# Optimization experiments

Hardware: AMD Instinct MI355X
Metric: run time of the kernel (lower is better)

The kernel has to match this reference:

```python
import jax, jax.numpy as jnp
import numpy as np

TOPK, NC, ALPHA, BETA, EPS = 13, 80, 1.0, 6.0, 1e-9


def make_anchors():
    # YOLOv8 anchor centers for a 640x640 image, strides 8/16/32 -> 8400 points
    pts = []
    for s in (8, 16, 32):
        n = 640 // s
        yv, xv = jnp.meshgrid(jnp.arange(n, dtype=jnp.float32) + 0.5,
                              jnp.arange(n, dtype=jnp.float32) + 0.5, indexing='ij')
        pts.append(jnp.stack([xv, yv], -1).reshape(-1, 2) * s)
    return jnp.concatenate(pts, 0)  # (8400, 2)


def setup_inputs() -> dict:
    key = jax.random.key(0)
    ks = jax.random.split(key, 5)
    B, NMAX = 32, 64
    anc_points = make_anchors()
    A = anc_points.shape[0]
    pd_scores = jax.random.uniform(ks[0], (B, A, NC), jnp.float32)
    # predicted boxes: anchor-centered xyxy with random extents
    half = jax.random.uniform(ks[1], (B, A, 2), jnp.float32) * 32.0 + 2.0
    ctr = anc_points[None]
    pd_bboxes = jnp.concatenate([ctr - half, ctr + half], -1)
    # gt boxes: valid xyxy inside the 640x640 image
    xy = jax.random.uniform(ks[2], (B, NMAX, 2), jnp.float32) * 520.0
    wh = jax.random.uniform(ks[3], (B, NMAX, 2), jnp.float32) * 120.0 + 8.0
    gt_bboxes = jnp.concatenate([xy, xy + wh], -1)
    gt_labels = jax.random.randint(ks[4], (B, NMAX, 1), 0, NC).astype(jnp.int64)
    mask_gt = jnp.ones((B, NMAX, 1), jnp.float32)
    return {"pd_scores": pd_scores, "pd_bboxes": pd_bboxes, "anc_points": anc_points,
            "gt_labels": gt_labels, "gt_bboxes": gt_bboxes, "mask_gt": mask_gt}


def _iou_xyxy(box1, box2, eps=1e-7):
    # box1: (B, N, 1, 4), box2: (B, 1, A, 4) -> iou (B, N, A)
    lt = jnp.maximum(box1[..., :2], box2[..., :2])
    rb = jnp.minimum(box1[..., 2:], box2[..., 2:])
    wh = jnp.clip(rb - lt, 0.0)
    inter = wh[..., 0] * wh[..., 1]
    a1 = (box1[..., 2] - box1[..., 0]) * (box1[..., 3] - box1[..., 1])
    a2 = (box2[..., 2] - box2[..., 0]) * (box2[..., 3] - box2[..., 1])
    return inter / (a1 + a2 - inter + eps)


def reference(pd_scores, pd_bboxes, anc_points, gt_labels, gt_bboxes, mask_gt):
    B, A, _ = pd_scores.shape
    N = gt_bboxes.shape[1]
    # --- select_candidates_in_gts: anchor center strictly inside gt box ---
    deltas = jnp.concatenate([
        anc_points[None, None] - gt_bboxes[:, :, None, :2],
        gt_bboxes[:, :, None, 2:] - anc_points[None, None]], -1)  # (B,N,A,4)
    mask_in_gts = (deltas.min(-1) > EPS).astype(jnp.float32)       # (B,N,A)
    mask_valid = mask_in_gts * mask_gt                             # mask_gt (B,N,1)
    # --- get_box_metrics ---
    # bbox_scores[b,n,a] = pd_scores[b, a, gt_labels[b,n]]
    bbox_scores = jnp.take_along_axis(pd_scores.transpose(0, 2, 1),
                                      gt_labels, axis=1)           # (B,N,A)
    overlaps = jnp.clip(_iou_xyxy(gt_bboxes[:, :, None], pd_bboxes[:, None]), 0.0)
    align_metric = (bbox_scores ** ALPHA) * (overlaps ** BETA)
    align_metric = align_metric * mask_valid
    overlaps = overlaps * mask_valid
    # --- select_topk_candidates ---
    _, topk_idxs = jax.lax.top_k(align_metric, TOPK)               # (B,N,TOPK)
    bi = jnp.arange(B)[:, None, None]
    ni = jnp.arange(N)[None, :, None]
    mask_topk = jnp.zeros_like(align_metric).at[bi, ni, topk_idxs].set(1.0)
    mask_pos = mask_valid * mask_topk                              # (B,N,A)
    fg_mask = mask_pos.sum(1)                                      # (B,A)
    # multi-GT conflict resolution (always applied; no-op when no conflicts)
    max_metric = align_metric.max(1, keepdims=True)
    mask_pos = jnp.where(fg_mask[:, None, :] > 1,
                         mask_pos * (align_metric == max_metric).astype(mask_pos.dtype),
                         mask_pos)
    fg_mask = mask_pos.sum(1)
    target_gt_idx = jnp.argmax(mask_pos, 1)                        # (B,A)
    # --- targets ---
    b2 = jnp.arange(B)[:, None]
    target_labels = gt_labels[..., 0][b2, target_gt_idx]           # (B,A)
    target_bboxes = gt_bboxes[b2, target_gt_idx]                   # (B,A,4)
    pos_align = (align_metric * mask_pos).max(1)                   # (B,A)
    target_scores = jax.nn.one_hot(target_labels, NC, dtype=jnp.float32) \
        * pos_align[..., None]                                     # (B,A,NC)
    return (target_bboxes, target_scores, fg_mask.astype(bool))
```

## Files before the change

kernel.cpp:

```cpp
#include <hip/hip_runtime.h>

#define BB 32
#define AA 8400
#define NGT 64
#define NCLS 80
#define TOPK 13
#define SLOTS 5
#define CHUNK 256
#define NCHUNK 33

__device__ __forceinline__ void anchor_xy(int a, float& px, float& py) {
    if (a < 6400)      { int y = a / 80;          int x = a - 80 * y;  px = (x + 0.5f) * 8.0f;  py = (y + 0.5f) * 8.0f; }
    else if (a < 8000) { int r = a - 6400; int y = r / 40; int x = r - 40 * y; px = (x + 0.5f) * 16.0f; py = (y + 0.5f) * 16.0f; }
    else               { int r = a - 8000; int y = r / 20; int x = r - 20 * y; px = (x + 0.5f) * 32.0f; py = (y + 0.5f) * 32.0f; }
}

__global__ __launch_bounds__(256) void k_topk(
    const float* __restrict__ pd_scores,
    const float4* __restrict__ pd_bboxes,
    const int* __restrict__ gt_labels,
    const float4* __restrict__ gt_bboxes,
    const float* __restrict__ mask_gt,
    int* __restrict__ list)
{
    __shared__ unsigned long long keys[4 * TOPK];
    int tid = threadIdx.x;
    int w = tid >> 6, lane = tid & 63;
    int gid = blockIdx.x * 2 + (w >> 1);
    int half = w & 1;
    int b = gid >> 6;

    if (tid < 4 * TOPK) keys[tid] = 0;
    __syncthreads();

    float4 g = gt_bboxes[gid];
    int label = gt_labels[gid];
    float ga1 = (g.z - g.x) * (g.w - g.y);
    bool valid = mask_gt[gid] > 0.0f;

    float va[SLOTS]; int ai[SLOTS]; int cnt = 0;
    #pragma unroll
    for (int j = 0; j < SLOTS; ++j) { va[j] = -1.0f; ai[j] = -1; }

#define SCAN_LEVEL(S, N, OFF)                                                   \
    {                                                                           \
        const float inv = 1.0f / (float)(S);                                    \
        int xlo = (int)floorf(g.x * inv - 0.5f); if (xlo < 0) xlo = 0;          \
        int xhi = (int)ceilf (g.z * inv - 0.5f); if (xhi > (N)-1) xhi = (N)-1;  \
        int ylo = (int)floorf(g.y * inv - 0.5f); if (ylo < 0) ylo = 0;          \
        int yhi = (int)ceilf (g.w * inv - 0.5f); if (yhi > (N)-1) yhi = (N)-1;  \
        int nx = xhi - xlo + 1, ny = yhi - ylo + 1;                             \
        int tot = (nx > 0 && ny > 0) ? nx * ny : 0;                             \
        for (int c = half * 64 + lane; c < tot; c += 128) {                     \
            int yy = c / nx, xx = c - yy * nx;                                  \
            int gx = xlo + xx, gy = ylo + yy;                                   \
            int a = (OFF) + gy * (N) + gx;                                      \
            float px = (gx + 0.5f) * (float)(S), py = (gy + 0.5f) * (float)(S); \
            float dmin = fminf(fminf(px - g.x, py - g.y),                       \
                               fminf(g.z - px, g.w - py));                      \
            if (dmin > 1e-9f) {                                                 \
                float4 pb = pd_bboxes[b * AA + a];                              \
                float ltx = fmaxf(g.x, pb.x), lty = fmaxf(g.y, pb.y);           \
                float rbx = fminf(g.z, pb.z), rby = fminf(g.w, pb.w);           \
                float wd = fmaxf(rbx - ltx, 0.0f), hg = fmaxf(rby - lty, 0.0f); \
                float inter = wd * hg;                                          \
                float a2 = (pb.z - pb.x) * (pb.w - pb.y);                       \
                float iou = fmaxf(inter / (ga1 + a2 - inter + 1e-7f), 0.0f);    \
                float sc = pd_scores[(size_t)(b * AA + a) * NCLS + label];      \
                float i2 = iou * iou;                                           \
                float v = sc * (i2 * i2 * i2);                                  \
                if (v > 0.0f) {                                                 \
                    _Pragma("unroll")                                           \
                    for (int j = 0; j < SLOTS; ++j)                             \
                        if (j == cnt) { va[j] = v; ai[j] = a; }                 \
                    cnt++;                                                      \
                }                                                               \
            }                                                                   \
        }                                                                       \
    }

    if (valid) {
        SCAN_LEVEL(8, 80, 0)
        SCAN_LEVEL(16, 40, 6400)
        SCAN_LEVEL(32, 20, 8000)
    }
#undef SCAN_LEVEL

    for (int k = 0; k < TOPK; ++k) {
        unsigned long long key = 0;
        #pragma unroll
        for (int j = 0; j < SLOTS; ++j)
            if (va[j] > 0.0f) {
                unsigned long long kk =
                    ((unsigned long long)__float_as_uint(va[j]) << 32)
                    | (unsigned)(0x7FFFFFFF - ai[j]);
                key = kk > key ? kk : key;
            }
        #pragma unroll
        for (int off = 32; off; off >>= 1) {
            unsigned long long o = __shfl_xor(key, off);
            key = o > key ? o : key;
        }
        if (key == 0) break;
        if (lane == 0) keys[w * TOPK + k] = key;
        int wa = 0x7FFFFFFF - (int)(unsigned)(key & 0xFFFFFFFFull);
        #pragma unroll
        for (int j = 0; j < SLOTS; ++j) if (ai[j] == wa) va[j] = -1.0f;
    }

    __syncthreads();

    if (!(w & 1)) {
        unsigned long long mykey = (lane < 2 * TOPK) ? keys[w * TOPK + lane] : 0;
        int kc = 0;
        for (int k = 0; k < TOPK; ++k) {
            unsigned long long best = mykey;
            #pragma unroll
            for (int off = 32; off; off >>= 1) {
                unsigned long long o = __shfl_xor(best, off);
                best = o > best ? o : best;
            }
            if (best == 0) break;
            if (lane == 0)
                list[gid * 16 + k] = 0x7FFFFFFF - (int)(unsigned)(best & 0xFFFFFFFFull);
            kc++;
            if (mykey == best) mykey = 0;
        }
        if (lane == 0)
            for (int k = kc; k < 16; ++k) list[gid * 16 + k] = -1;
    }
}

__global__ __launch_bounds__(256) void k_out(
    const float* __restrict__ pd_scores,
    const float4* __restrict__ pd_bboxes,
    const int* __restrict__ gt_labels,
    const float4* __restrict__ gt_bboxes,
    const float* __restrict__ mask_gt,
    const int* __restrict__ list,
    float4* __restrict__ out_bbox,
    float* __restrict__ out_fg,
    float4* __restrict__ out_scores)
{
    __shared__ unsigned int s_lo[CHUNK], s_hi[CHUNK];
    __shared__ float4 s_gt[NGT];
    __shared__ int    s_glab[NGT];
    __shared__ float  s_gmsk[NGT];

    int bidx = blockIdx.x;
    int b = bidx / NCHUNK;
    int chunk = bidx - b * NCHUNK;
    int abase = chunk * CHUNK;
    int count = AA - abase; if (count > CHUNK) count = CHUNK;
    int tid = threadIdx.x;

    float4* dst = out_scores + (size_t)(b * AA + abase) * (NCLS / 4);
    const float4 z4 = make_float4(0.f, 0.f, 0.f, 0.f);
    for (int ci = tid; ci < count * (NCLS / 4); ci += 256)
        dst[ci] = z4;

    s_lo[tid] = 0; s_hi[tid] = 0;
    if (tid < NGT) {
        s_gt[tid]   = gt_bboxes[b * NGT + tid];
        s_glab[tid] = gt_labels[b * NGT + tid];
        s_gmsk[tid] = mask_gt[b * NGT + tid];
    }
    __syncthreads();

    const int* blist = list + b * NGT * 16;
    for (int e = tid; e < NGT * 16; e += 256) {
        int a = blist[e];
        int rel = a - abase;
        if (a >= 0 && rel >= 0 && rel < count) {
            int n = e >> 4;
            if (n < 32) atomicOr(&s_lo[rel], 1u << n);
            else        atomicOr(&s_hi[rel], 1u << (n - 32));
        }
    }
    __syncthreads();

    if (tid < count) {
        int a = abase + tid;
        int idx = b * AA + a;
        unsigned long long m = ((unsigned long long)s_hi[tid] << 32) | s_lo[tid];
        float pos = 0.0f; int tgt = 0; int fg = 0;
        if (m) {
            float px, py; anchor_xy(a, px, py);
            float4 pb = pd_bboxes[idx];
            float a2 = (pb.z - pb.x) * (pb.w - pb.y);
            if (__popcll(m) == 1) {
                int n = __ffsll((unsigned long long)m) - 1;
                float4 gg = s_gt[n];
                float ltx = fmaxf(gg.x, pb.x), lty = fmaxf(gg.y, pb.y);
                float rbx = fminf(gg.z, pb.z), rby = fminf(gg.w, pb.w);
                float wd = fmaxf(rbx - ltx, 0.0f), hg = fmaxf(rby - lty, 0.0f);
                float inter = wd * hg;
                float a1 = (gg.z - gg.x) * (gg.w - gg.y);
                float iou = fmaxf(inter / (a1 + a2 - inter + 1e-7f), 0.0f);
                float sc = pd_scores[(size_t)idx * NCLS + s_glab[n]];
                float i2 = iou * iou;
                pos = sc * (i2 * i2 * i2);
                tgt = n; fg = 1;
            } else {
                float mmax = 0.0f; unsigned long long nb = 0;
                for (int j0 = 0; j0 < NGT; j0 += 8) {
                    float v[8];
                    #pragma unroll
                    for (int j = 0; j < 8; ++j) {
                        int n = j0 + j;
                        float4 gg = s_gt[n];
                        float sc = pd_scores[(size_t)idx * NCLS + s_glab[n]];
                        float dmin = fminf(fminf(px - gg.x, py - gg.y),
                                           fminf(gg.z - px, gg.w - py));
                        float ltx = fmaxf(gg.x, pb.x), lty = fmaxf(gg.y, pb.y);
                        float rbx = fminf(gg.z, pb.z), rby = fminf(gg.w, pb.w);
                        float wd = fmaxf(rbx - ltx, 0.0f), hg = fmaxf(rby - lty, 0.0f);
                        float inter = wd * hg;
                        float a1 = (gg.z - gg.x) * (gg.w - gg.y);
                        float iou = fmaxf(inter / (a1 + a2 - inter + 1e-7f), 0.0f);
                        float i2 = iou * iou;
                        bool ok = (s_gmsk[n] > 0.0f) && (dmin > 1e-9f);
                        v[j] = ok ? sc * (i2 * i2 * i2) : 0.0f;
                    }
                    #pragma unroll
                    for (int j = 0; j < 8; ++j) {
                        int n = j0 + j;
                        float vv = v[j];
                        if (vv > mmax) { mmax = vv; nb = m & (1ull << n); }
                        else if (vv == mmax && vv > 0.0f) nb |= m & (1ull << n);
                    }
                }
                if (nb) { tgt = __ffsll(nb) - 1; pos = mmax; fg = 1; }
            }
        }
        out_bbox[idx] = s_gt[tgt];
        out_fg[idx] = fg ? 1.0f : 0.0f;
        if (fg && pos != 0.0f)
            ((float*)dst)[(size_t)tid * NCLS + s_glab[tgt]] = pos;
    }
}

extern "C" void kernel_launch(void* const* d_in, const int* in_sizes, int n_in,
                              void* d_out, int out_size, void* d_ws, size_t ws_size,
                              hipStream_t stream) {
    const float*  pd_scores = (const float*) d_in[0];
    const float4* pd_bboxes = (const float4*)d_in[1];
    const int*    gt_labels = (const int*)   d_in[3];
    const float4* gt_bboxes = (const float4*)d_in[4];
    const float*  mask_gt   = (const float*) d_in[5];

    float* out = (float*)d_out;
    float4* out_bbox   = (float4*)out;
    float4* out_scores = (float4*)(out + (size_t)BB * AA * 4);
    float*  out_fg     = out + (size_t)BB * AA * 4 + (size_t)BB * AA * NCLS;

    int* list = (int*)d_ws;

    k_topk<<<BB * NGT / 2, 256, 0, stream>>>(pd_scores, pd_bboxes,
                                             gt_labels, gt_bboxes, mask_gt, list);

    k_out<<<BB * NCHUNK, 256, 0, stream>>>(
        pd_scores, pd_bboxes, gt_labels, gt_bboxes, mask_gt, list,
        out_bbox, out_fg, out_scores);
}
```

Before: 68.71 us.

## Move output zero-fill to a separate kernel and scatter top-k hits as global bitmasks

A new fill kernel zeroes the scores, fg and bitmask buffers and writes default bboxes up front. The top-k kernel now atomically ORs each selected GT's bit into a per-anchor 64-bit mask in global memory, replacing the per-GT candidate list. The resolve kernel reads that mask directly and exits early for anchors with no hits, which removes the per-block list scan and shared-memory atomics. The trade-off is an extra kernel launch, a full-size zero pass over the large score tensor in a kernel separate from the resolve work, and global atomics.

```diff
diff --git a/kernel.cpp b/kernel.cpp
--- a/kernel.cpp
+++ b/kernel.cpp
@@ -15,20 +15,36 @@
     else               { int r = a - 8000; int y = r / 20; int x = r - 20 * y; px = (x + 0.5f) * 32.0f; py = (y + 0.5f) * 32.0f; }
 }
 
+__global__ __launch_bounds__(256) void k_fill(
+    float4* __restrict__ scores4,
+    float4* __restrict__ fg4,
+    float4* __restrict__ bbox4,
+    float4* __restrict__ bits4,
+    const float4* __restrict__ gt_bboxes)
+{
+    const int nthr = gridDim.x * 256;
+    int gtid = blockIdx.x * 256 + threadIdx.x;
+    const float4 z4 = make_float4(0.f, 0.f, 0.f, 0.f);
+    for (int j = gtid; j < BB * AA * (NCLS / 4); j += nthr) scores4[j] = z4;
+    for (int j = gtid; j < BB * AA / 4;          j += nthr) fg4[j] = z4;
+    for (int j = gtid; j < BB * AA / 2;          j += nthr) bits4[j] = z4;
+    for (int j = gtid; j < BB * AA;              j += nthr) bbox4[j] = gt_bboxes[(j / AA) << 6];
+}
+
 __global__ __launch_bounds__(256) void k_topk(
     const float* __restrict__ pd_scores,
     const float4* __restrict__ pd_bboxes,
     const int* __restrict__ gt_labels,
     const float4* __restrict__ gt_bboxes,
     const float* __restrict__ mask_gt,
-    int* __restrict__ list)
+    unsigned long long* __restrict__ bits)
 {
     __shared__ unsigned long long keys[4 * TOPK];
     int tid = threadIdx.x;
     int w = tid >> 6, lane = tid & 63;
     int gid = blockIdx.x * 2 + (w >> 1);
     int half = w & 1;
-    int b = gid >> 6;
+    int b = gid >> 6, n = gid & 63;
 
     if (tid < 4 * TOPK) keys[tid] = 0;
     __syncthreads();
@@ -112,7 +128,8 @@
 
     if (!(w & 1)) {
         unsigned long long mykey = (lane < 2 * TOPK) ? keys[w * TOPK + lane] : 0;
-        int kc = 0;
+        unsigned long long* mybits = bits + (size_t)b * AA;
+        unsigned long long nbit = 1ull << n;
         for (int k = 0; k < TOPK; ++k) {
             unsigned long long best = mykey;
             #pragma unroll
@@ -121,28 +138,26 @@
                 best = o > best ? o : best;
             }
             if (best == 0) break;
-            if (lane == 0)
-                list[gid * 16 + k] = 0x7FFFFFFF - (int)(unsigned)(best & 0xFFFFFFFFull);
-            kc++;
+            if (lane == 0) {
+                int wa = 0x7FFFFFFF - (int)(unsigned)(best & 0xFFFFFFFFull);
+                atomicOr(&mybits[wa], nbit);
+            }
             if (mykey == best) mykey = 0;
         }
-        if (lane == 0)
-            for (int k = kc; k < 16; ++k) list[gid * 16 + k] = -1;
-    }
-}
-
-__global__ __launch_bounds__(256) void k_out(
+    }
+}
+
+__global__ __launch_bounds__(256) void k_resolve(
     const float* __restrict__ pd_scores,
     const float4* __restrict__ pd_bboxes,
     const int* __restrict__ gt_labels,
     const float4* __restrict__ gt_bboxes,
     const float* __restrict__ mask_gt,
-    const int* __restrict__ list,
+    const unsigned long long* __restrict__ bits,
     float4* __restrict__ out_bbox,
     float* __restrict__ out_fg,
-    float4* __restrict__ out_scores)
+    float* __restrict__ out_scores)
 {
-    __shared__ unsigned int s_lo[CHUNK], s_hi[CHUNK];
     __shared__ float4 s_gt[NGT];
     __shared__ int    s_glab[NGT];
     __shared__ float  s_gmsk[NGT];
@@ -154,12 +169,6 @@
     int count = AA - abase; if (count > CHUNK) count = CHUNK;
     int tid = threadIdx.x;
 
-    float4* dst = out_scores + (size_t)(b * AA + abase) * (NCLS / 4);
-    const float4 z4 = make_float4(0.f, 0.f, 0.f, 0.f);
-    for (int ci = tid; ci < count * (NCLS / 4); ci += 256)
-        dst[ci] = z4;
-
-    s_lo[tid] = 0; s_hi[tid] = 0;
     if (tid < NGT) {
         s_gt[tid]   = gt_bboxes[b * NGT + tid];
         s_glab[tid] = gt_labels[b * NGT + tid];
@@ -167,77 +176,64 @@
     }
     __syncthreads();
 
-    const int* blist = list + b * NGT * 16;
-    for (int e = tid; e < NGT * 16; e += 256) {
-        int a = blist[e];
-        int rel = a - abase;
-        if (a >= 0 && rel >= 0 && rel < count) {
-            int n = e >> 4;
-            if (n < 32) atomicOr(&s_lo[rel], 1u << n);
-            else        atomicOr(&s_hi[rel], 1u << (n - 32));
-        }
-    }
-    __syncthreads();
-
-    if (tid < count) {
-        int a = abase + tid;
-        int idx = b * AA + a;
-        unsigned long long m = ((unsigned long long)s_hi[tid] << 32) | s_lo[tid];
-        float pos = 0.0f; int tgt = 0; int fg = 0;
-        if (m) {
-            float px, py; anchor_xy(a, px, py);
-            float4 pb = pd_bboxes[idx];
-            float a2 = (pb.z - pb.x) * (pb.w - pb.y);
-            if (__popcll(m) == 1) {
-                int n = __ffsll((unsigned long long)m) - 1;
+    if (tid >= count) return;
+    int a = abase + tid;
+    int idx = b * AA + a;
+    unsigned long long m = bits[idx];
+    if (!m) return;
+
+    float px, py; anchor_xy(a, px, py);
+    float4 pb = pd_bboxes[idx];
+    float a2 = (pb.z - pb.x) * (pb.w - pb.y);
+    float pos = 0.0f; int tgt = 0;
+    if (__popcll(m) == 1) {
+        int n = __ffsll((unsigned long long)m) - 1;
+        float4 gg = s_gt[n];
+        float ltx = fmaxf(gg.x, pb.x), lty = fmaxf(gg.y, pb.y);
+        float rbx = fminf(gg.z, pb.z), rby = fminf(gg.w, pb.w);
+        float wd = fmaxf(rbx - ltx, 0.0f), hg = fmaxf(rby - lty, 0.0f);
+        float inter = wd * hg;
+        float a1 = (gg.z - gg.x) * (gg.w - gg.y);
+        float iou = fmaxf(inter / (a1 + a2 - inter + 1e-7f), 0.0f);
+        float sc = pd_scores[(size_t)idx * NCLS + s_glab[n]];
+        float i2 = iou * iou;
+        pos = sc * (i2 * i2 * i2);
+        tgt = n;
+    } else {
+        float mmax = 0.0f; unsigned long long nb = 0;
+        for (int j0 = 0; j0 < NGT; j0 += 8) {
+            float v[8];
+            #pragma unroll
+            for (int j = 0; j < 8; ++j) {
+                int n = j0 + j;
                 float4 gg = s_gt[n];
+                float sc = pd_scores[(size_t)idx * NCLS + s_glab[n]];
+                float dmin = fminf(fminf(px - gg.x, py - gg.y),
+                                   fminf(gg.z - px, gg.w - py));
                 float ltx = fmaxf(gg.x, pb.x), lty = fmaxf(gg.y, pb.y);
                 float rbx = fminf(gg.z, pb.z), rby = fminf(gg.w, pb.w);
                 float wd = fmaxf(rbx - ltx, 0.0f), hg = fmaxf(rby - lty, 0.0f);
                 float inter = wd * hg;
                 float a1 = (gg.z - gg.x) * (gg.w - gg.y);
                 float iou = fmaxf(inter / (a1 + a2 - inter + 1e-7f), 0.0f);
-                float sc = pd_scores[(size_t)idx * NCLS + s_glab[n]];
                 float i2 = iou * iou;
-                pos = sc * (i2 * i2 * i2);
-                tgt = n; fg = 1;
-            } else {
-                float mmax = 0.0f; unsigned long long nb = 0;
-                for (int j0 = 0; j0 < NGT; j0 += 8) {
-                    float v[8];
-                    #pragma unroll
-                    for (int j = 0; j < 8; ++j) {
-                        int n = j0 + j;
-                        float4 gg = s_gt[n];
-                        float sc = pd_scores[(size_t)idx * NCLS + s_glab[n]];
-                        float dmin = fminf(fminf(px - gg.x, py - gg.y),
-                                           fminf(gg.z - px, gg.w - py));
-                        float ltx = fmaxf(gg.x, pb.x), lty = fmaxf(gg.y, pb.y);
-                        float rbx = fminf(gg.z, pb.z), rby = fminf(gg.w, pb.w);
-                        float wd = fmaxf(rbx - ltx, 0.0f), hg = fmaxf(rby - lty, 0.0f);
-                        float inter = wd * hg;
-                        float a1 = (gg.z - gg.x) * (gg.w - gg.y);
-                        float iou = fmaxf(inter / (a1 + a2 - inter + 1e-7f), 0.0f);
-                        float i2 = iou * iou;
-                        bool ok = (s_gmsk[n] > 0.0f) && (dmin > 1e-9f);
-                        v[j] = ok ? sc * (i2 * i2 * i2) : 0.0f;
-                    }
-                    #pragma unroll
-                    for (int j = 0; j < 8; ++j) {
-                        int n = j0 + j;
-                        float vv = v[j];
-                        if (vv > mmax) { mmax = vv; nb = m & (1ull << n); }
-                        else if (vv == mmax && vv > 0.0f) nb |= m & (1ull << n);
-                    }
-                }
-                if (nb) { tgt = __ffsll(nb) - 1; pos = mmax; fg = 1; }
+                bool ok = (s_gmsk[n] > 0.0f) && (dmin > 1e-9f);
+                v[j] = ok ? sc * (i2 * i2 * i2) : 0.0f;
+            }
+            #pragma unroll
+            for (int j = 0; j < 8; ++j) {
+                int n = j0 + j;
+                float vv = v[j];
+                if (vv > mmax) { mmax = vv; nb = m & (1ull << n); }
+                else if (vv == mmax && vv > 0.0f) nb |= m & (1ull << n);
             }
         }
-        out_bbox[idx] = s_gt[tgt];
-        out_fg[idx] = fg ? 1.0f : 0.0f;
-        if (fg && pos != 0.0f)
-            ((float*)dst)[(size_t)tid * NCLS + s_glab[tgt]] = pos;
-    }
+        if (!nb) return;
+        tgt = __ffsll(nb) - 1; pos = mmax;
+    }
+    out_bbox[idx] = s_gt[tgt];
+    out_fg[idx] = 1.0f;
+    out_scores[(size_t)idx * NCLS + s_glab[tgt]] = pos;
 }
 
 extern "C" void kernel_launch(void* const* d_in, const int* in_sizes, int n_in,
@@ -251,15 +247,18 @@
 
     float* out = (float*)d_out;
     float4* out_bbox   = (float4*)out;
-    float4* out_scores = (float4*)(out + (size_t)BB * AA * 4);
+    float*  out_scores = out + (size_t)BB * AA * 4;
     float*  out_fg     = out + (size_t)BB * AA * 4 + (size_t)BB * AA * NCLS;
 
-    int* list = (int*)d_ws;
+    unsigned long long* bits = (unsigned long long*)d_ws;
+
+    k_fill<<<2048, 256, 0, stream>>>(
+        (float4*)out_scores, (float4*)out_fg, out_bbox, (float4*)bits, gt_bboxes);
 
     k_topk<<<BB * NGT / 2, 256, 0, stream>>>(pd_scores, pd_bboxes,
-                                             gt_labels, gt_bboxes, mask_gt, list);
-
-    k_out<<<BB * NCHUNK, 256, 0, stream>>>(
-        pd_scores, pd_bboxes, gt_labels, gt_bboxes, mask_gt, list,
+                                             gt_labels, gt_bboxes, mask_gt, bits);
+
+    k_resolve<<<BB * NCHUNK, 256, 0, stream>>>(
+        pd_scores, pd_bboxes, gt_labels, gt_bboxes, mask_gt, bits,
         out_bbox, out_fg, out_scores);
 }
```

After: 77.29 us. +12.5%, slower.

## Split score writing into separate dense one-hot kernel via workspace

Applied to the files above, without the earlier changes.

Moves the target_scores writing out of the resolve kernel. The resolve kernel now stores the per-anchor positive value and label into workspace, and a new elementwise kernel writes each float4 of the (B,A,80) score tensor once, with the value placed in the label slot. This replaces a zero-fill followed by a scattered store with one fully coalesced write pass. It costs an extra kernel launch and a small workspace round-trip.

```diff
diff --git a/kernel.cpp b/kernel.cpp
--- a/kernel.cpp
+++ b/kernel.cpp
@@ -131,7 +131,7 @@
     }
 }
 
-__global__ __launch_bounds__(256) void k_out(
+__global__ __launch_bounds__(256) void k_resolve(
     const float* __restrict__ pd_scores,
     const float4* __restrict__ pd_bboxes,
     const int* __restrict__ gt_labels,
@@ -140,7 +140,8 @@
     const int* __restrict__ list,
     float4* __restrict__ out_bbox,
     float* __restrict__ out_fg,
-    float4* __restrict__ out_scores)
+    float* __restrict__ ws_pos,
+    int* __restrict__ ws_lab)
 {
     __shared__ unsigned int s_lo[CHUNK], s_hi[CHUNK];
     __shared__ float4 s_gt[NGT];
@@ -153,11 +154,6 @@
     int abase = chunk * CHUNK;
     int count = AA - abase; if (count > CHUNK) count = CHUNK;
     int tid = threadIdx.x;
-
-    float4* dst = out_scores + (size_t)(b * AA + abase) * (NCLS / 4);
-    const float4 z4 = make_float4(0.f, 0.f, 0.f, 0.f);
-    for (int ci = tid; ci < count * (NCLS / 4); ci += 256)
-        dst[ci] = z4;
 
     s_lo[tid] = 0; s_hi[tid] = 0;
     if (tid < NGT) {
@@ -179,65 +175,85 @@
     }
     __syncthreads();
 
-    if (tid < count) {
-        int a = abase + tid;
-        int idx = b * AA + a;
-        unsigned long long m = ((unsigned long long)s_hi[tid] << 32) | s_lo[tid];
-        float pos = 0.0f; int tgt = 0; int fg = 0;
-        if (m) {
-            float px, py; anchor_xy(a, px, py);
-            float4 pb = pd_bboxes[idx];
-            float a2 = (pb.z - pb.x) * (pb.w - pb.y);
-            if (__popcll(m) == 1) {
-                int n = __ffsll((unsigned long long)m) - 1;
-                float4 gg = s_gt[n];
-                float ltx = fmaxf(gg.x, pb.x), lty = fmaxf(gg.y, pb.y);
-                float rbx = fminf(gg.z, pb.z), rby = fminf(gg.w, pb.w);
-                float wd = fmaxf(rbx - ltx, 0.0f), hg = fmaxf(rby - lty, 0.0f);
-                float inter = wd * hg;
-                float a1 = (gg.z - gg.x) * (gg.w - gg.y);
-                float iou = fmaxf(inter / (a1 + a2 - inter + 1e-7f), 0.0f);
-                float sc = pd_scores[(size_t)idx * NCLS + s_glab[n]];
-                float i2 = iou * iou;
-                pos = sc * (i2 * i2 * i2);
-                tgt = n; fg = 1;
-            } else {
-                float mmax = 0.0f; unsigned long long nb = 0;
-                for (int j0 = 0; j0 < NGT; j0 += 8) {
-                    float v[8];
-                    #pragma unroll
-                    for (int j = 0; j < 8; ++j) {
-                        int n = j0 + j;
-                        float4 gg = s_gt[n];
-                        float sc = pd_scores[(size_t)idx * NCLS + s_glab[n]];
-                        float dmin = fminf(fminf(px - gg.x, py - gg.y),
-                                           fminf(gg.z - px, gg.w - py));
-                        float ltx = fmaxf(gg.x, pb.x), lty = fmaxf(gg.y, pb.y);
-                        float rbx = fminf(gg.z, pb.z), rby = fminf(gg.w, pb.w);
-                        float wd = fmaxf(rbx - ltx, 0.0f), hg = fmaxf(rby - lty, 0.0f);
-                        float inter = wd * hg;
-                        float a1 = (gg.z - gg.x) * (gg.w - gg.y);
-                        float iou = fmaxf(inter / (a1 + a2 - inter + 1e-7f), 0.0f);
-                        float i2 = iou * iou;
-                        bool ok = (s_gmsk[n] > 0.0f) && (dmin > 1e-9f);
-                        v[j] = ok ? sc * (i2 * i2 * i2) : 0.0f;
-                    }
-                    #pragma unroll
-                    for (int j = 0; j < 8; ++j) {
-                        int n = j0 + j;
-                        float vv = v[j];
-                        if (vv > mmax) { mmax = vv; nb = m & (1ull << n); }
-                        else if (vv == mmax && vv > 0.0f) nb |= m & (1ull << n);
-                    }
+    if (tid >= count) return;
+    int a = abase + tid;
+    int idx = b * AA + a;
+    unsigned long long m = ((unsigned long long)s_hi[tid] << 32) | s_lo[tid];
+    float pos = 0.0f; int tgt = 0; int fg = 0;
+    if (m) {
+        float px, py; anchor_xy(a, px, py);
+        float4 pb = pd_bboxes[idx];
+        float a2 = (pb.z - pb.x) * (pb.w - pb.y);
+        if (__popcll(m) == 1) {
+            int n = __ffsll((unsigned long long)m) - 1;
+            float4 gg = s_gt[n];
+            float ltx = fmaxf(gg.x, pb.x), lty = fmaxf(gg.y, pb.y);
+            float rbx = fminf(gg.z, pb.z), rby = fminf(gg.w, pb.w);
+            float wd = fmaxf(rbx - ltx, 0.0f), hg = fmaxf(rby - lty, 0.0f);
+            float inter = wd * hg;
+            float a1 = (gg.z - gg.x) * (gg.w - gg.y);
+            float iou = fmaxf(inter / (a1 + a2 - inter + 1e-7f), 0.0f);
+            float sc = pd_scores[(size_t)idx * NCLS + s_glab[n]];
+            float i2 = iou * iou;
+            pos = sc * (i2 * i2 * i2);
+            tgt = n; fg = 1;
+        } else {
+            float mmax = 0.0f; unsigned long long nb = 0;
+            for (int j0 = 0; j0 < NGT; j0 += 8) {
+                float v[8];
+                #pragma unroll
+                for (int j = 0; j < 8; ++j) {
+                    int n = j0 + j;
+                    float4 gg = s_gt[n];
+                    float sc = pd_scores[(size_t)idx * NCLS + s_glab[n]];
+                    float dmin = fminf(fminf(px - gg.x, py - gg.y),
+                                       fminf(gg.z - px, gg.w - py));
+                    float ltx = fmaxf(gg.x, pb.x), lty = fmaxf(gg.y, pb.y);
+                    float rbx = fminf(gg.z, pb.z), rby = fminf(gg.w, pb.w);
+                    float wd = fmaxf(rbx - ltx, 0.0f), hg = fmaxf(rby - lty, 0.0f);
+                    float inter = wd * hg;
+                    float a1 = (gg.z - gg.x) * (gg.w - gg.y);
+                    float iou = fmaxf(inter / (a1 + a2 - inter + 1e-7f), 0.0f);
+                    float i2 = iou * iou;
+                    bool ok = (s_gmsk[n] > 0.0f) && (dmin > 1e-9f);
+                    v[j] = ok ? sc * (i2 * i2 * i2) : 0.0f;
                 }
-                if (nb) { tgt = __ffsll(nb) - 1; pos = mmax; fg = 1; }
+                #pragma unroll
+                for (int j = 0; j < 8; ++j) {
+                    int n = j0 + j;
+                    float vv = v[j];
+                    if (vv > mmax) { mmax = vv; nb = m & (1ull << n); }
+                    else if (vv == mmax && vv > 0.0f) nb |= m & (1ull << n);
+                }
             }
-        }
-        out_bbox[idx] = s_gt[tgt];
-        out_fg[idx] = fg ? 1.0f : 0.0f;
-        if (fg && pos != 0.0f)
-            ((float*)dst)[(size_t)tid * NCLS + s_glab[tgt]] = pos;
-    }
+            if (nb) { tgt = __ffsll(nb) - 1; pos = mmax; fg = 1; }
+            else    { pos = 0.0f; tgt = 0; fg = 0; }
+        }
+    }
+    out_bbox[idx] = s_gt[tgt];
+    out_fg[idx] = fg ? 1.0f : 0.0f;
+    ws_pos[idx] = fg ? pos : 0.0f;
+    ws_lab[idx] = s_glab[tgt];
+}
+
+__global__ __launch_bounds__(256) void k_scores(
+    const float* __restrict__ ws_pos,
+    const int* __restrict__ ws_lab,
+    float4* __restrict__ out_scores)
+{
+    int t = blockIdx.x * 256 + threadIdx.x;
+    int anchor = t / (NCLS / 4);
+    int c0 = (t - anchor * (NCLS / 4)) * 4;
+    float pos = ws_pos[anchor];
+    int lab = ws_lab[anchor];
+    float4 r = make_float4(0.0f, 0.0f, 0.0f, 0.0f);
+    if (pos != 0.0f) {
+        if (lab == c0)     r.x = pos;
+        if (lab == c0 + 1) r.y = pos;
+        if (lab == c0 + 2) r.z = pos;
+        if (lab == c0 + 3) r.w = pos;
+    }
+    out_scores[t] = r;
 }
 
 extern "C" void kernel_launch(void* const* d_in, const int* in_sizes, int n_in,
@@ -251,15 +267,20 @@
 
     float* out = (float*)d_out;
     float4* out_bbox   = (float4*)out;
-    float4* out_scores = (float4*)(out + (size_t)BB * AA * 4);
+    float*  out_scores = out + (size_t)BB * AA * 4;
     float*  out_fg     = out + (size_t)BB * AA * 4 + (size_t)BB * AA * NCLS;
 
-    int* list = (int*)d_ws;
+    int*   list   = (int*)d_ws;
+    float* ws_pos = (float*)((char*)d_ws + 131072);
+    int*   ws_lab = (int*)  ((char*)d_ws + 131072 + BB * AA * 4);
 
     k_topk<<<BB * NGT / 2, 256, 0, stream>>>(pd_scores, pd_bboxes,
                                              gt_labels, gt_bboxes, mask_gt, list);
 
-    k_out<<<BB * NCHUNK, 256, 0, stream>>>(
+    k_resolve<<<BB * NCHUNK, 256, 0, stream>>>(
         pd_scores, pd_bboxes, gt_labels, gt_bboxes, mask_gt, list,
-        out_bbox, out_fg, out_scores);
-}
+        out_bbox, out_fg, ws_pos, ws_lab);
+
+    k_scores<<<BB * AA * (NCLS / 4) / 256, 256, 0, stream>>>(
+        ws_pos, ws_lab, (float4*)out_scores);
+}
```

New measurement: 75.96 us. +10.5%, slower.
